# Performance work log

Measured on AMD Instinct MI355X. Metric: run time of the kernel, lower is better.

Reference implementation:

```python
import jax, jax.numpy as jnp
import numpy as np

D = 128        # dim_features
I = 3          # num_iterations (forward uses I+1 slices)
P = 64         # num_projections
Q = 100        # num_quantiles
G = 1000       # number of graphs in the batch
N = 200000     # total nodes
POW = 2        # p of the p-sliced Wasserstein


def setup_inputs() -> dict:
    key = jax.random.key(0)
    k1, k2, k3 = jax.random.split(key, 3)
    x = jax.random.normal(k1, (N, (I + 1) * D), dtype=jnp.float32)
    batch = jnp.sort(jax.random.randint(k2, (N,), 0, G, dtype=jnp.int32))
    proj = jax.random.normal(k3, (D, P), dtype=jnp.float32)
    proj = proj / jnp.sqrt(jnp.sum(proj ** 2, axis=0, keepdims=True))
    cum_weights = jnp.linspace(0.0, 1.0, Q, dtype=jnp.float32)
    return {"x": x, "batch": batch, "projections": proj, "cum_weights": cum_weights}


def reference(x, batch, projections, cum_weights):
    n = x.shape[0]
    # project all WL iterations at once: [N, I+1, D] @ [D, P] -> [N, I+1, P]
    xp = jnp.einsum('nid,dp->nip', x.reshape(n, I + 1, D), projections)

    # segment bookkeeping (batch is sorted, segments contiguous)
    counts = jax.ops.segment_sum(jnp.ones((n,), jnp.int32), batch, num_segments=G)
    starts = jnp.cumsum(counts) - counts  # exclusive prefix sum
    # torch.quantile(..., interpolation='lower'): index = floor(q * (len-1))
    qidx = starts[:, None] + jnp.floor(
        cum_weights[None, :] * jnp.maximum(counts - 1, 0)[:, None].astype(cum_weights.dtype)
    ).astype(jnp.int32)  # [G, Q]

    # segmented sort: per column, lexsort by (batch primary, value secondary)
    def sort_col(v):  # v: [N]
        order = jnp.lexsort((v, batch))
        return v[order]

    flat = xp.reshape(n, (I + 1) * P)
    sorted_vals = jax.vmap(sort_col, in_axes=1, out_axes=1)(flat)  # [N, (I+1)*P]

    quant = sorted_vals[qidx]                       # [G, Q, (I+1)*P]
    quant = quant.reshape(G, Q, I + 1, P)
    quant = jnp.transpose(quant, (0, 2, 1, 3))       # [G, I+1, Q, P] (torch flattens [Q,P] Q-major, concat over i)
    scale = (Q * P) ** (1.0 / POW)
    return (quant / scale).reshape(G, (I + 1) * Q * P)
```

## Files before the change

kernel.cpp:

```cpp
#include <hip/hip_runtime.h>
#include <cstdint>
#include <cstddef>

#define NN 200000
#define DD 128
#define II 4
#define PP 64
#define QQ 100
#define GG 1000

__global__ void starts_kernel(const int* __restrict__ batch, int* __restrict__ starts) {
    int g = blockIdx.x * blockDim.x + threadIdx.x;
    if (g > GG) return;
    if (g == GG) { starts[g] = NN; return; }
    int lo = 0, hi = NN;
    while (lo < hi) {
        int mid = (lo + hi) >> 1;
        if (batch[mid] < g) lo = mid + 1; else hi = mid;
    }
    starts[g] = lo;
}

__global__ __launch_bounds__(256) void proj_kernel(
        const float* __restrict__ x, const float* __restrict__ proj,
        float* __restrict__ xp) {
    __shared__ float xs[64 * 132];
    const int t    = threadIdx.x;
    const int n0   = blockIdx.x * 64;
    const int i    = blockIdx.y;
    const int lane = t & 63;
    const int pg   = __builtin_amdgcn_readfirstlane(t >> 6);

    {
        const int c4 = t & 31;
        const int r0 = t >> 5;
        #pragma unroll
        for (int pass = 0; pass < 8; ++pass) {
            const int row = r0 + pass * 8;
            const float4 v = *(const float4*)(x + (size_t)(n0 + row) * 512 + i * 128 + c4 * 4);
            *(float4*)(xs + row * 132 + c4 * 4) = v;
        }
    }
    __syncthreads();

    float acc[16];
    #pragma unroll
    for (int pp = 0; pp < 16; ++pp) acc[pp] = 0.f;

    const float* __restrict__ pbase = proj + pg * 16;
    const float* __restrict__ xrow  = xs + lane * 132;

    #pragma unroll 4
    for (int d4 = 0; d4 < 32; ++d4) {
        const float4 xv = *(const float4*)(xrow + d4 * 4);
        #pragma unroll
        for (int pp = 0; pp < 16; ++pp) acc[pp] += xv.x * pbase[(d4 * 4 + 0) * 64 + pp];
        #pragma unroll
        for (int pp = 0; pp < 16; ++pp) acc[pp] += xv.y * pbase[(d4 * 4 + 1) * 64 + pp];
        #pragma unroll
        for (int pp = 0; pp < 16; ++pp) acc[pp] += xv.z * pbase[(d4 * 4 + 2) * 64 + pp];
        #pragma unroll
        for (int pp = 0; pp < 16; ++pp) acc[pp] += xv.w * pbase[(d4 * 4 + 3) * 64 + pp];
    }

    float* __restrict__ obase = xp + ((size_t)i * 64 + pg * 16) * NN + n0 + lane;
    #pragma unroll
    for (int pp = 0; pp < 16; ++pp)
        obase[(size_t)pp * NN] = acc[pp];
}

template<int VPT>
__device__ inline void bitonic_sort(float v[VPT], int lane) {
    constexpr int NS = VPT * 64;
    #pragma unroll
    for (int k = 2; k <= NS; k <<= 1) {
        #pragma unroll
        for (int j = k >> 1; j >= 1; j >>= 1) {
            if (j >= VPT) {
                const int  d        = j / VPT;
                const bool up       = ((lane * VPT) & k) == 0;
                const bool lower    = (lane & d) == 0;
                const bool keep_min = (up == lower);
                #pragma unroll
                for (int r = 0; r < VPT; ++r) {
                    const float pv = __shfl_xor(v[r], d);
                    v[r] = ((pv < v[r]) == keep_min) ? pv : v[r];
                }
            } else {
                #pragma unroll
                for (int r = 0; r < VPT; ++r) {
                    if ((r & j) == 0) {
                        const int  r2 = r | j;
                        const bool up = (((lane * VPT + r) & k) == 0);
                        const float a = v[r], b = v[r2];
                        const bool sw = ((b < a) == up);
                        v[r]  = sw ? b : a;
                        v[r2] = sw ? a : b;
                    }
                }
            }
        }
    }
}

__global__ __launch_bounds__(512) void sort_quant_kernel(
        const float* __restrict__ xp, const int* __restrict__ starts,
        const float* __restrict__ cw, float* __restrict__ out) {
    __shared__ float sbuf[8 * 516];
    const int b    = blockIdx.x;
    const int g    = b >> 3;
    const int pq   = b & 7;
    const int i    = blockIdx.y;
    const int t    = threadIdx.x;
    const int w    = __builtin_amdgcn_readfirstlane(t >> 6);
    const int lane = t & 63;

    const int start = starts[g];
    const int cnt   = starts[g + 1] - start;

    const int col = pq * 8 + w;
    const float* __restrict__ src = xp + ((size_t)i * 64 + col) * NN + start;
    float* lrow = sbuf + w * 516;

    if (cnt <= 256) {
        float v[4];
        #pragma unroll
        for (int r = 0; r < 4; ++r) {
            const int e = lane * 4 + r;
            v[r] = (e < cnt) ? src[e] : __builtin_inff();
        }
        bitonic_sort<4>(v, lane);
        *(float4*)(lrow + lane * 4) = make_float4(v[0], v[1], v[2], v[3]);
    } else {
        float v[8];
        #pragma unroll
        for (int r = 0; r < 8; ++r) {
            const int e = lane * 8 + r;
            v[r] = (e < cnt && e < 512) ? src[e] : __builtin_inff();
        }
        bitonic_sort<8>(v, lane);
        *(float4*)(lrow + lane * 8)     = make_float4(v[0], v[1], v[2], v[3]);
        *(float4*)(lrow + lane * 8 + 4) = make_float4(v[4], v[5], v[6], v[7]);
    }
    __syncthreads();

    const float cm1 = (float)(cnt > 0 ? cnt - 1 : 0);
    const int   pl  = t & 7;
    const int   qt  = t >> 3;
    const float inv_scale = 1.0f / 80.0f;
    float* __restrict__ orow = out + (size_t)g * 25600 + i * 6400 + pq * 8 + pl;

    {
        const int q  = qt;
        int tq = (int)floorf(cw[q] * cm1);
        if (tq > 511) tq = 511;
        orow[q * 64] = sbuf[pl * 516 + tq] * inv_scale;
    }
    if (qt < QQ - 64) {
        const int q  = 64 + qt;
        int tq = (int)floorf(cw[q] * cm1);
        if (tq > 511) tq = 511;
        orow[q * 64] = sbuf[pl * 516 + tq] * inv_scale;
    }
}

extern "C" void kernel_launch(void* const* d_in, const int* in_sizes, int n_in,
                              void* d_out, int out_size, void* d_ws, size_t ws_size,
                              hipStream_t stream) {
    const float* x     = (const float*)d_in[0];
    const int*   batch = (const int*)  d_in[1];
    const float* proj  = (const float*)d_in[2];
    const float* cw    = (const float*)d_in[3];
    float*       out   = (float*)d_out;

    int*   starts = (int*)d_ws;
    float* xp     = (float*)((char*)d_ws + 4096);

    starts_kernel<<<4, 256, 0, stream>>>(batch, starts);
    proj_kernel<<<dim3(NN / 64, II), 256, 0, stream>>>(x, proj, xp);
    sort_quant_kernel<<<dim3(GG * 8, II), 512, 0, stream>>>(xp, starts, cw, out);
}
```

Measured before the change: 880.5 us.

## Replace bitonic sort with flip-merge network using DPP cross-lane ops

Rewrites the per-wavefront sort as a sorting network whose first stage of each merge is a reversed (flip) comparison, so every compare-exchange has a fixed direction. In-register exchanges become plain min/max, and cross-lane exchanges use DPP or ds_swizzle moves instead of generic shuffles, with the keep-min choice taken from a compile-time lane mask in inline asm. This removes the per-element direction arithmetic and the costly bpermute shuffles. The cost is inline asm that clobbers vcc and code tied to the wave64 DPP encodings.

```diff
diff --git a/kernel.cpp b/kernel.cpp
--- a/kernel.cpp
+++ b/kernel.cpp
@@ -69,38 +69,93 @@
         obase[(size_t)pp * NN] = acc[pp];
 }
 
+constexpr uint64_t lanebit_mask(int B) {
+    uint64_t m = 0;
+    for (int l = 0; l < 64; ++l) if ((l & B) == 0) m |= (1ull << l);
+    return m;
+}
+
+__device__ __forceinline__ float cx_sel(float vr, float pv, uint64_t km) {
+    float out;
+    asm("v_cmp_lt_f32 vcc, %1, %2\n\t"
+        "s_xnor_b64 vcc, vcc, %3\n\t"
+        "v_cndmask_b32 %0, %2, %1, vcc"
+        : "=v"(out)
+        : "v"(pv), "v"(vr), "s"(km)
+        : "vcc");
+    return out;
+}
+
+__device__ __forceinline__ void mm(float& a, float& b) {
+    const float mn = fminf(a, b), mx = fmaxf(a, b);
+    a = mn; b = mx;
+}
+
+template<int XM>
+__device__ __forceinline__ float xlane(float x) {
+    if constexpr (XM == 63) {
+        return __shfl_xor(x, 63, 64);
+    } else {
+        const int xi = __float_as_int(x);
+        int r;
+        if constexpr (XM == 1)       r = __builtin_amdgcn_mov_dpp(xi, 0xB1,  0xF, 0xF, false);
+        else if constexpr (XM == 2)  r = __builtin_amdgcn_mov_dpp(xi, 0x4E,  0xF, 0xF, false);
+        else if constexpr (XM == 3)  r = __builtin_amdgcn_mov_dpp(xi, 0x1B,  0xF, 0xF, false);
+        else if constexpr (XM == 7)  r = __builtin_amdgcn_mov_dpp(xi, 0x141, 0xF, 0xF, false);
+        else if constexpr (XM == 15) r = __builtin_amdgcn_mov_dpp(xi, 0x140, 0xF, 0xF, false);
+        else                         r = __builtin_amdgcn_ds_swizzle(xi, (XM << 10) | 0x1F);
+        return __int_as_float(r);
+    }
+}
+
+template<int VPT, int M>
+__device__ __forceinline__ void comp_stage(float (&v)[VPT]) {
+    if constexpr (M <= VPT) {
+        #pragma unroll
+        for (int b = 0; b < VPT; b += M) {
+            #pragma unroll
+            for (int p = 0; p < M / 2; ++p) {
+                mm(v[b + p], v[b + M - 1 - p]);
+            }
+        }
+    } else {
+        constexpr int LX = M / VPT - 1;
+        constexpr int B  = (LX + 1) >> 1;
+        constexpr uint64_t km = lanebit_mask(B);
+        float pv[VPT];
+        #pragma unroll
+        for (int r = 0; r < VPT; ++r) pv[r] = xlane<LX>(v[(VPT - 1) ^ r]);
+        #pragma unroll
+        for (int r = 0; r < VPT; ++r) v[r] = cx_sel(v[r], pv[r], km);
+    }
+}
+
+template<int VPT, int J>
+__device__ __forceinline__ void clean_stage(float (&v)[VPT]) {
+    if constexpr (J >= VPT) {
+        constexpr int D = J / VPT;
+        constexpr uint64_t km = lanebit_mask(D);
+        #pragma unroll
+        for (int r = 0; r < VPT; ++r) v[r] = cx_sel(v[r], xlane<D>(v[r]), km);
+    } else {
+        #pragma unroll
+        for (int r = 0; r < VPT; ++r) {
+            if ((r & J) == 0) mm(v[r], v[r | J]);
+        }
+    }
+    if constexpr (J > 1) clean_stage<VPT, J / 2>(v);
+}
+
+template<int VPT, int NS, int M>
+__device__ __forceinline__ void msort(float (&v)[VPT]) {
+    comp_stage<VPT, M>(v);
+    if constexpr (M >= 4) clean_stage<VPT, M / 4>(v);
+    if constexpr (M < NS) msort<VPT, NS, M * 2>(v);
+}
+
 template<int VPT>
-__device__ inline void bitonic_sort(float v[VPT], int lane) {
-    constexpr int NS = VPT * 64;
-    #pragma unroll
-    for (int k = 2; k <= NS; k <<= 1) {
-        #pragma unroll
-        for (int j = k >> 1; j >= 1; j >>= 1) {
-            if (j >= VPT) {
-                const int  d        = j / VPT;
-                const bool up       = ((lane * VPT) & k) == 0;
-                const bool lower    = (lane & d) == 0;
-                const bool keep_min = (up == lower);
-                #pragma unroll
-                for (int r = 0; r < VPT; ++r) {
-                    const float pv = __shfl_xor(v[r], d);
-                    v[r] = ((pv < v[r]) == keep_min) ? pv : v[r];
-                }
-            } else {
-                #pragma unroll
-                for (int r = 0; r < VPT; ++r) {
-                    if ((r & j) == 0) {
-                        const int  r2 = r | j;
-                        const bool up = (((lane * VPT + r) & k) == 0);
-                        const float a = v[r], b = v[r2];
-                        const bool sw = ((b < a) == up);
-                        v[r]  = sw ? b : a;
-                        v[r2] = sw ? a : b;
-                    }
-                }
-            }
-        }
-    }
+__device__ __forceinline__ void bitonic_sort(float (&v)[VPT]) {
+    msort<VPT, VPT * 64, 2>(v);
 }
 
 __global__ __launch_bounds__(512) void sort_quant_kernel(
@@ -129,7 +184,7 @@
             const int e = lane * 4 + r;
             v[r] = (e < cnt) ? src[e] : __builtin_inff();
         }
-        bitonic_sort<4>(v, lane);
+        bitonic_sort<4>(v);
         *(float4*)(lrow + lane * 4) = make_float4(v[0], v[1], v[2], v[3]);
     } else {
         float v[8];
@@ -138,7 +193,7 @@
             const int e = lane * 8 + r;
             v[r] = (e < cnt && e < 512) ? src[e] : __builtin_inff();
         }
-        bitonic_sort<8>(v, lane);
+        bitonic_sort<8>(v);
         *(float4*)(lrow + lane * 8)     = make_float4(v[0], v[1], v[2], v[3]);
         *(float4*)(lrow + lane * 8 + 4) = make_float4(v[4], v[5], v[6], v[7]);
     }
```

Result: faster. 804.5 us (-8.6%).
